# Kernel optimization log

Measured on AMD Instinct MI355X. Metric: run time of the kernel, lower is better.

## Reference

```python
import jax, jax.numpy as jnp
import numpy as np

D_MODEL = 1024
N_HEADS = 16
HEAD_DIM = D_MODEL // N_HEADS
ROPE_BASE = 10000.0


def setup_inputs() -> dict:
    key = jax.random.key(0)
    ks = jax.random.split(key, 5)
    B, S = 2, 2048
    x = jax.random.normal(ks[0], (B, S, D_MODEL), dtype=jnp.float32)
    scale = 1.0 / np.sqrt(D_MODEL)
    Wq = jax.random.normal(ks[1], (D_MODEL, D_MODEL), dtype=jnp.float32) * scale
    Wk = jax.random.normal(ks[2], (D_MODEL, D_MODEL), dtype=jnp.float32) * scale
    Wv = jax.random.normal(ks[3], (D_MODEL, D_MODEL), dtype=jnp.float32) * scale
    Wo = jax.random.normal(ks[4], (D_MODEL, D_MODEL), dtype=jnp.float32) * scale
    return {"x": x, "Wq": Wq, "Wk": Wk, "Wv": Wv, "Wo": Wo}


def _rope_cos_sin(seq_len, dtype):
    # inv_freq over half the head dim, duplicated (cat[freqs, freqs])
    inv_freq = 1.0 / (ROPE_BASE ** (jnp.arange(0, HEAD_DIM, 2, dtype=jnp.float32) / HEAD_DIM))
    t = jnp.arange(seq_len, dtype=jnp.float32)
    freqs = jnp.outer(t, inv_freq)                 # [S, HD/2]
    emb = jnp.concatenate([freqs, freqs], axis=-1)  # [S, HD]
    return jnp.cos(emb).astype(dtype), jnp.sin(emb).astype(dtype)


def _rotate_half(v):
    v1, v2 = jnp.split(v, 2, axis=-1)
    return jnp.concatenate([-v2, v1], axis=-1)


def reference(x, Wq, Wk, Wv, Wo):
    B, S, _ = x.shape
    # torch Linear: y = x @ W.T  (weights stored [out, in])
    def proj(W):
        y = jnp.einsum('bsd,ed->bse', x, W)
        return y.reshape(B, S, N_HEADS, HEAD_DIM).transpose(0, 2, 1, 3)  # [B,H,S,HD]
    q, k, v = proj(Wq), proj(Wk), proj(Wv)

    cos, sin = _rope_cos_sin(S, x.dtype)  # [S, HD]
    cos = cos[None, None]                 # [1,1,S,HD]
    sin = sin[None, None]
    q = q * cos + _rotate_half(q) * sin
    k = k * cos + _rotate_half(k) * sin

    scale = 1.0 / np.sqrt(HEAD_DIM)
    scores = jnp.einsum('bhqd,bhkd->bhqk', q, k) * scale  # [B,H,S,S]
    causal = jnp.triu(jnp.ones((S, S), dtype=bool), k=1)
    scores = jnp.where(causal, jnp.finfo(scores.dtype).min, scores)
    attn = jax.nn.softmax(scores, axis=-1)
    out = jnp.einsum('bhqk,bhkd->bhqd', attn, v)          # [B,H,S,HD]
    out = out.transpose(0, 2, 1, 3).reshape(B, S, D_MODEL)
    return jnp.einsum('bsd,ed->bse', out, Wo)
```

## Files before the change

### kernel.cpp

```cpp
#include <hip/hip_runtime.h>

typedef unsigned short u16;
typedef __attribute__((ext_vector_type(8))) short short8;
typedef __attribute__((ext_vector_type(4))) float floatx4;

#define D_MODEL 1024
#define NHEADS 16
#define HD 64
#define BATCH 2
#define SEQ 2048
#define MROWS (BATCH * SEQ)

static __device__ __forceinline__ u16 f2bf(float f) {
  unsigned int u = __float_as_uint(f);
  u += 0x7fffu + ((u >> 16) & 1u);
  return (u16)(u >> 16);
}

__global__ void cvt_all(const float* __restrict__ x, const float* __restrict__ wq,
                        const float* __restrict__ wk, const float* __restrict__ wv,
                        const float* __restrict__ wo, u16* __restrict__ xb,
                        u16* __restrict__ wqkvb, u16* __restrict__ wob) {
  const int i = blockIdx.x * 256 + threadIdx.x;
  const int chunk = i >> 18;
  const float* src;
  u16* dst;
  int loc;
  switch (chunk) {
    case 0: case 1: case 2: case 3: src = x;  dst = xb;              loc = i;              break;
    case 4:                          src = wq; dst = wqkvb;           loc = i - (4 << 18); break;
    case 5:                          src = wk; dst = wqkvb + 1048576; loc = i - (5 << 18); break;
    case 6:                          src = wv; dst = wqkvb + 2097152; loc = i - (6 << 18); break;
    default:                         src = wo; dst = wob;             loc = i - (7 << 18); break;
  }
  const float4 v = ((const float4*)src)[loc];
  ushort4 o;
  o.x = f2bf(v.x); o.y = f2bf(v.y); o.z = f2bf(v.z); o.w = f2bf(v.w);
  ((ushort4*)dst)[loc] = o;
}

__global__ __launch_bounds__(256) void gemm_qkv(
    const u16* __restrict__ A, const u16* __restrict__ B,
    u16* __restrict__ qb, u16* __restrict__ kb, u16* __restrict__ vb, int K) {
  __shared__ u16 As[128 * 32];
  __shared__ u16 Bs[128 * 32];
  const int t = threadIdx.x;
  const int lane = t & 63;
  const int wv = t >> 6;
  const int wr = wv >> 1, wc = wv & 1;
  const int m0 = blockIdx.y * 128, n0 = blockIdx.x * 128;
  const int qd = lane >> 4, lr = lane & 15;
  const int arow = lane >> 2;
  const int acol = (lane & 3) * 8;

  floatx4 acc[4][4];
#pragma unroll
  for (int i = 0; i < 4; ++i)
#pragma unroll
    for (int j = 0; j < 4; ++j) acc[i][j] = (floatx4){0.f, 0.f, 0.f, 0.f};

  for (int kt = 0; kt < K; kt += 32) {
    __syncthreads();
#pragma unroll
    for (int i = 0; i < 2; ++i) {
      const int seg = wv * 2 + i;
      const u16* ga = &A[(size_t)(m0 + seg * 16 + arow) * K + kt + acol];
      const u16* gb = &B[(size_t)(n0 + seg * 16 + arow) * K + kt + acol];
      __builtin_amdgcn_global_load_lds(
          (const __attribute__((address_space(1))) void*)ga,
          (__attribute__((address_space(3))) void*)&As[seg * 512], 16, 0, 0);
      __builtin_amdgcn_global_load_lds(
          (const __attribute__((address_space(1))) void*)gb,
          (__attribute__((address_space(3))) void*)&Bs[seg * 512], 16, 0, 0);
    }
    __syncthreads();

    short8 af[4], bfr[4];
#pragma unroll
    for (int i = 0; i < 4; ++i)
      af[i] = *(const short8*)&As[(wr * 64 + i * 16 + lr) * 32 + qd * 8];
#pragma unroll
    for (int j = 0; j < 4; ++j)
      bfr[j] = *(const short8*)&Bs[(wc * 64 + j * 16 + lr) * 32 + qd * 8];
#pragma unroll
    for (int i = 0; i < 4; ++i)
#pragma unroll
      for (int j = 0; j < 4; ++j)
        acc[i][j] = __builtin_amdgcn_mfma_f32_16x16x32_bf16(af[i], bfr[j], acc[i][j], 0, 0, 0);
  }

  const int tn = n0 >> 10;
  if (tn == 2) {
#pragma unroll
    for (int i = 0; i < 4; ++i) {
      const int mb = m0 + wr * 64 + i * 16 + qd * 4;
      const int b = mb >> 11, s = mb & 2047;
#pragma unroll
      for (int j = 0; j < 4; ++j) {
        const int nn = (n0 + wc * 64 + j * 16 + lr) & 1023;
        const int h = nn >> 6, d = nn & 63;
        ushort4 o;
        o.x = f2bf(acc[i][j][0]); o.y = f2bf(acc[i][j][1]);
        o.z = f2bf(acc[i][j][2]); o.w = f2bf(acc[i][j][3]);
        *(ushort4*)&vb[((size_t)(b * NHEADS + h) * HD + d) * SEQ + s] = o;
      }
    }
  } else {
    u16* dst = (tn == 0) ? qb : kb;
    const float qs = (tn == 0) ? 0.18033688011112042f : 1.0f;
    const int h = ((n0 & 1023) >> 6) + wc;
    const float inv0 = __builtin_exp2f(-(float)lr * 0.4152410118609203f);
    const float inv1 = __builtin_exp2f(-(float)(lr + 16) * 0.4152410118609203f);
#pragma unroll
    for (int i = 0; i < 4; ++i) {
      const int mb = m0 + wr * 64 + i * 16 + qd * 4;
      const int b = mb >> 11;
      const size_t rowbase = (size_t)(b * NHEADS + h) * SEQ;
#pragma unroll
      for (int r = 0; r < 4; ++r) {
        const int sq = (mb + r) & 2047;
        float s0, c0, s1, c1;
        __sincosf((float)sq * inv0, &s0, &c0);
        __sincosf((float)sq * inv1, &s1, &c1);
#pragma unroll
        for (int j = 0; j < 4; ++j) {
          const float v = acc[i][j][r];
          const float pv = acc[i][j ^ 2][r];
          const float cc = (j & 1) ? c1 : c0;
          const float ss = (j & 1) ? s1 : s0;
          const float res = (v * cc + ((j < 2) ? -pv : pv) * ss) * qs;
          dst[(rowbase + sq) * HD + j * 16 + lr] = f2bf(res);
        }
      }
    }
  }
}

__global__ __launch_bounds__(256) void gemm_out(
    const u16* __restrict__ A, const u16* __restrict__ B, float* __restrict__ fo,
    int N, int K) {
  __shared__ u16 As[64 * 32];
  __shared__ u16 Bs[128 * 32];
  const int t = threadIdx.x;
  const int lane = t & 63, wv = t >> 6;
  const int m0 = blockIdx.y * 64, n0 = blockIdx.x * 128;
  const int qd = lane >> 4, lr = lane & 15;
  const int arow = lane >> 2;
  const int acol = (lane & 3) * 8;

  floatx4 acc[8];
#pragma unroll
  for (int j = 0; j < 8; ++j) acc[j] = (floatx4){0.f, 0.f, 0.f, 0.f};

  for (int kt = 0; kt < K; kt += 32) {
    __syncthreads();
    {
      const u16* ga = &A[(size_t)(m0 + wv * 16 + arow) * K + kt + acol];
      __builtin_amdgcn_global_load_lds(
          (const __attribute__((address_space(1))) void*)ga,
          (__attribute__((address_space(3))) void*)&As[wv * 512], 16, 0, 0);
#pragma unroll
      for (int i = 0; i < 2; ++i) {
        const int seg = wv * 2 + i;
        const u16* gb = &B[(size_t)(n0 + seg * 16 + arow) * K + kt + acol];
        __builtin_amdgcn_global_load_lds(
            (const __attribute__((address_space(1))) void*)gb,
            (__attribute__((address_space(3))) void*)&Bs[seg * 512], 16, 0, 0);
      }
    }
    __syncthreads();
    const short8 af = *(const short8*)&As[(wv * 16 + lr) * 32 + qd * 8];
#pragma unroll
    for (int j = 0; j < 8; ++j) {
      const short8 bfr = *(const short8*)&Bs[(j * 16 + lr) * 32 + qd * 8];
      acc[j] = __builtin_amdgcn_mfma_f32_16x16x32_bf16(af, bfr, acc[j], 0, 0, 0);
    }
  }
#pragma unroll
  for (int j = 0; j < 8; ++j)
#pragma unroll
    for (int r = 0; r < 4; ++r)
      fo[(size_t)(m0 + wv * 16 + qd * 4 + r) * N + n0 + j * 16 + lr] = acc[j][r];
}

__global__ __launch_bounds__(256, 2) void flash_mfma(
    const u16* __restrict__ Q, const u16* __restrict__ Kg,
    const u16* __restrict__ Vg, u16* __restrict__ O) {
  __shared__ u16 Ks[2][2][64 * 32];
  __shared__ u16 Vs[2][2][64 * 32];
  __shared__ u16 Ps[4][2][16][72];
  const int t = threadIdx.x;
  const int lane = t & 63, wv = t >> 6;
  const int lr = lane & 15, qd = lane >> 4;
  const int bh = blockIdx.x;
  const int y = (int)blockIdx.y;
  const int c = (y < 8) ? (15 - y) : (y - 8);
  const int nsteps = 2 * c + 2;
  const int q0w = c * 128 + wv * 32;
  const size_t baseQK = (size_t)bh * SEQ * HD;
  const size_t baseV = (size_t)bh * HD * SEQ;
  const int b = bh >> 4, h = bh & 15;
  const int srow = lane >> 2;
  const int scol = (lane & 3) * 8;

  auto stage = [&](int buf, int k0) {
    const int hh = wv & 1;
    if (wv < 2) {
#pragma unroll
      for (int seg = 0; seg < 4; ++seg) {
        const u16* g = &Kg[baseQK + (size_t)(k0 + seg * 16 + srow) * HD + hh * 32 + scol];
        __builtin_amdgcn_global_load_lds(
            (const __attribute__((address_space(1))) void*)g,
            (__attribute__((address_space(3))) void*)&Ks[buf][hh][seg * 512], 16, 0, 0);
      }
    } else {
#pragma unroll
      for (int seg = 0; seg < 4; ++seg) {
        const u16* g = &Vg[baseV + (size_t)(seg * 16 + srow) * SEQ + k0 + hh * 32 + scol];
        __builtin_amdgcn_global_load_lds(
            (const __attribute__((address_space(1))) void*)g,
            (__attribute__((address_space(3))) void*)&Vs[buf][hh][seg * 512], 16, 0, 0);
      }
    }
  };

  short8 qf[2][2];
#pragma unroll
  for (int i = 0; i < 2; ++i)
#pragma unroll
    for (int s = 0; s < 2; ++s)
      qf[i][s] = *(const short8*)&Q[baseQK + (size_t)(q0w + i * 16 + lr) * HD + s * 32 + qd * 8];

  float l_i[2] = {0.f, 0.f};
  floatx4 oacc[2][4];
#pragma unroll
  for (int i = 0; i < 2; ++i)
#pragma unroll
    for (int dj = 0; dj < 4; ++dj) oacc[i][dj] = (floatx4){0.f, 0.f, 0.f, 0.f};

  stage(0, 0);

  for (int kt = 0; kt < nsteps; ++kt) {
    __syncthreads();
    if (kt + 1 < nsteps) stage((kt + 1) & 1, (kt + 1) * 64);
    const int k0 = kt * 64;
    if (k0 > q0w + 31) continue;
    const int buf = kt & 1;

    short8 kf[2][4], vf[2][4];
#pragma unroll
    for (int s = 0; s < 2; ++s)
#pragma unroll
      for (int jj = 0; jj < 4; ++jj)
        kf[s][jj] = *(const short8*)&Ks[buf][s][(jj * 16 + lr) * 32 + qd * 8];
#pragma unroll
    for (int s = 0; s < 2; ++s)
#pragma unroll
      for (int dj = 0; dj < 4; ++dj)
        vf[s][dj] = *(const short8*)&Vs[buf][s][(dj * 16 + lr) * 32 + qd * 8];

    floatx4 sv[2][4];
#pragma unroll
    for (int i = 0; i < 2; ++i)
#pragma unroll
      for (int jj = 0; jj < 4; ++jj) sv[i][jj] = (floatx4){0.f, 0.f, 0.f, 0.f};
#pragma unroll
    for (int s = 0; s < 2; ++s)
#pragma unroll
      for (int jj = 0; jj < 4; ++jj) {
        sv[1][jj] = __builtin_amdgcn_mfma_f32_16x16x32_bf16(kf[s][jj], qf[1][s], sv[1][jj], 0, 0, 0);
        sv[0][jj] = __builtin_amdgcn_mfma_f32_16x16x32_bf16(kf[s][jj], qf[0][s], sv[0][jj], 0, 0, 0);
      }

#pragma unroll
    for (int i = 0; i < 2; ++i) {
      const int dq = (q0w + i * 16) - k0;
      if (dq < 63) {
#pragma unroll
        for (int jj = 0; jj < 4; ++jj)
#pragma unroll
          for (int r = 0; r < 4; ++r)
            if (jj * 16 + qd * 4 + r > dq + lr) sv[i][jj][r] = -1e30f;
      }
      float rs = 0.f;
#pragma unroll
      for (int jj = 0; jj < 4; ++jj) {
        const float p0 = __builtin_exp2f(sv[i][jj][0]);
        const float p1 = __builtin_exp2f(sv[i][jj][1]);
        const float p2 = __builtin_exp2f(sv[i][jj][2]);
        const float p3 = __builtin_exp2f(sv[i][jj][3]);
        rs += (p0 + p1) + (p2 + p3);
        uint2 pk;
        pk.x = __builtin_amdgcn_perm(__float_as_uint(p1), __float_as_uint(p0), 0x07060302);
        pk.y = __builtin_amdgcn_perm(__float_as_uint(p3), __float_as_uint(p2), 0x07060302);
        *(uint2*)&Ps[wv][i][lr][jj * 16 + qd * 4] = pk;
      }
      l_i[i] += rs;
    }

#pragma unroll
    for (int i = 0; i < 2; ++i) {
      const short8 pf0 = *(const short8*)&Ps[wv][i][lr][qd * 8];
      const short8 pf1 = *(const short8*)&Ps[wv][i][lr][32 + qd * 8];
#pragma unroll
      for (int dj = 0; dj < 4; ++dj)
        oacc[i][dj] = __builtin_amdgcn_mfma_f32_16x16x32_bf16(pf0, vf[0][dj], oacc[i][dj], 0, 0, 0);
#pragma unroll
      for (int dj = 0; dj < 4; ++dj)
        oacc[i][dj] = __builtin_amdgcn_mfma_f32_16x16x32_bf16(pf1, vf[1][dj], oacc[i][dj], 0, 0, 0);
    }
  }

#pragma unroll
  for (int i = 0; i < 2; ++i) {
    float lf = l_i[i];
    lf += __shfl_xor(lf, 16, 64);
    lf += __shfl_xor(lf, 32, 64);
#pragma unroll
    for (int r = 0; r < 4; ++r) {
      const float linv = 1.f / __shfl(lf, qd * 4 + r, 64);
      const int q = q0w + i * 16 + qd * 4 + r;
#pragma unroll
      for (int dj = 0; dj < 4; ++dj)
        O[(size_t)(b * SEQ + q) * D_MODEL + h * HD + dj * 16 + lr] = f2bf(oacc[i][dj][r] * linv);
    }
  }
}

extern "C" void kernel_launch(void* const* d_in, const int* in_sizes, int n_in,
                              void* d_out, int out_size, void* d_ws, size_t ws_size,
                              hipStream_t stream) {
  const float* x  = (const float*)d_in[0];
  const float* Wq = (const float*)d_in[1];
  const float* Wk = (const float*)d_in[2];
  const float* Wv = (const float*)d_in[3];
  const float* Wo = (const float*)d_in[4];
  float* out = (float*)d_out;

  u16* xb = (u16*)d_ws;
  u16* wqkv = xb + 4194304;
  u16* wo = wqkv + 3145728;
  u16* qb = wo + 1048576;
  u16* kb = qb + 4194304;
  u16* vb = kb + 4194304;
  u16* ow = vb + 4194304;

  cvt_all<<<8192, 256, 0, stream>>>(x, Wq, Wk, Wv, Wo, xb, wqkv, wo);
  gemm_qkv<<<dim3(24, 32), 256, 0, stream>>>(xb, wqkv, qb, kb, vb, 1024);
  flash_mfma<<<dim3(32, 16), 256, 0, stream>>>(qb, kb, vb, ow);
  gemm_out<<<dim3(8, 64), 256, 0, stream>>>(ow, wo, out, 1024, 1024);
}
```

Measured before the change: 186.6 us.

## Fuse all stages into one persistent kernel with atomic grid barriers

```diff
diff --git a/kernel.cpp b/kernel.cpp
--- a/kernel.cpp
+++ b/kernel.cpp
@@ -9,7 +9,7 @@
 #define HD 64
 #define BATCH 2
 #define SEQ 2048
-#define MROWS (BATCH * SEQ)
+#define NBLK 512u
 
 static __device__ __forceinline__ u16 f2bf(float f) {
   unsigned int u = __float_as_uint(f);
@@ -17,313 +17,318 @@
   return (u16)(u >> 16);
 }
 
-__global__ void cvt_all(const float* __restrict__ x, const float* __restrict__ wq,
-                        const float* __restrict__ wk, const float* __restrict__ wv,
-                        const float* __restrict__ wo, u16* __restrict__ xb,
-                        u16* __restrict__ wqkvb, u16* __restrict__ wob) {
-  const int i = blockIdx.x * 256 + threadIdx.x;
-  const int chunk = i >> 18;
-  const float* src;
-  u16* dst;
-  int loc;
-  switch (chunk) {
-    case 0: case 1: case 2: case 3: src = x;  dst = xb;              loc = i;              break;
-    case 4:                          src = wq; dst = wqkvb;           loc = i - (4 << 18); break;
-    case 5:                          src = wk; dst = wqkvb + 1048576; loc = i - (5 << 18); break;
-    case 6:                          src = wv; dst = wqkvb + 2097152; loc = i - (6 << 18); break;
-    default:                         src = wo; dst = wob;             loc = i - (7 << 18); break;
-  }
-  const float4 v = ((const float4*)src)[loc];
-  ushort4 o;
-  o.x = f2bf(v.x); o.y = f2bf(v.y); o.z = f2bf(v.z); o.w = f2bf(v.w);
-  ((ushort4*)dst)[loc] = o;
-}
-
-__global__ __launch_bounds__(256) void gemm_qkv(
-    const u16* __restrict__ A, const u16* __restrict__ B,
-    u16* __restrict__ qb, u16* __restrict__ kb, u16* __restrict__ vb, int K) {
-  __shared__ u16 As[128 * 32];
-  __shared__ u16 Bs[128 * 32];
-  const int t = threadIdx.x;
-  const int lane = t & 63;
-  const int wv = t >> 6;
-  const int wr = wv >> 1, wc = wv & 1;
-  const int m0 = blockIdx.y * 128, n0 = blockIdx.x * 128;
-  const int qd = lane >> 4, lr = lane & 15;
-  const int arow = lane >> 2;
-  const int acol = (lane & 3) * 8;
-
-  floatx4 acc[4][4];
-#pragma unroll
-  for (int i = 0; i < 4; ++i)
-#pragma unroll
-    for (int j = 0; j < 4; ++j) acc[i][j] = (floatx4){0.f, 0.f, 0.f, 0.f};
-
-  for (int kt = 0; kt < K; kt += 32) {
-    __syncthreads();
-#pragma unroll
-    for (int i = 0; i < 2; ++i) {
-      const int seg = wv * 2 + i;
-      const u16* ga = &A[(size_t)(m0 + seg * 16 + arow) * K + kt + acol];
-      const u16* gb = &B[(size_t)(n0 + seg * 16 + arow) * K + kt + acol];
-      __builtin_amdgcn_global_load_lds(
-          (const __attribute__((address_space(1))) void*)ga,
-          (__attribute__((address_space(3))) void*)&As[seg * 512], 16, 0, 0);
-      __builtin_amdgcn_global_load_lds(
-          (const __attribute__((address_space(1))) void*)gb,
-          (__attribute__((address_space(3))) void*)&Bs[seg * 512], 16, 0, 0);
-    }
-    __syncthreads();
-
-    short8 af[4], bfr[4];
-#pragma unroll
-    for (int i = 0; i < 4; ++i)
-      af[i] = *(const short8*)&As[(wr * 64 + i * 16 + lr) * 32 + qd * 8];
-#pragma unroll
-    for (int j = 0; j < 4; ++j)
-      bfr[j] = *(const short8*)&Bs[(wc * 64 + j * 16 + lr) * 32 + qd * 8];
-#pragma unroll
-    for (int i = 0; i < 4; ++i)
-#pragma unroll
-      for (int j = 0; j < 4; ++j)
-        acc[i][j] = __builtin_amdgcn_mfma_f32_16x16x32_bf16(af[i], bfr[j], acc[i][j], 0, 0, 0);
-  }
-
-  const int tn = n0 >> 10;
-  if (tn == 2) {
-#pragma unroll
-    for (int i = 0; i < 4; ++i) {
-      const int mb = m0 + wr * 64 + i * 16 + qd * 4;
-      const int b = mb >> 11, s = mb & 2047;
-#pragma unroll
-      for (int j = 0; j < 4; ++j) {
-        const int nn = (n0 + wc * 64 + j * 16 + lr) & 1023;
-        const int h = nn >> 6, d = nn & 63;
-        ushort4 o;
-        o.x = f2bf(acc[i][j][0]); o.y = f2bf(acc[i][j][1]);
-        o.z = f2bf(acc[i][j][2]); o.w = f2bf(acc[i][j][3]);
-        *(ushort4*)&vb[((size_t)(b * NHEADS + h) * HD + d) * SEQ + s] = o;
-      }
-    }
-  } else {
-    u16* dst = (tn == 0) ? qb : kb;
-    const float qs = (tn == 0) ? 0.18033688011112042f : 1.0f;
-    const int h = ((n0 & 1023) >> 6) + wc;
-    const float inv0 = __builtin_exp2f(-(float)lr * 0.4152410118609203f);
-    const float inv1 = __builtin_exp2f(-(float)(lr + 16) * 0.4152410118609203f);
-#pragma unroll
-    for (int i = 0; i < 4; ++i) {
-      const int mb = m0 + wr * 64 + i * 16 + qd * 4;
-      const int b = mb >> 11;
-      const size_t rowbase = (size_t)(b * NHEADS + h) * SEQ;
-#pragma unroll
-      for (int r = 0; r < 4; ++r) {
-        const int sq = (mb + r) & 2047;
-        float s0, c0, s1, c1;
-        __sincosf((float)sq * inv0, &s0, &c0);
-        __sincosf((float)sq * inv1, &s1, &c1);
-#pragma unroll
-        for (int j = 0; j < 4; ++j) {
-          const float v = acc[i][j][r];
-          const float pv = acc[i][j ^ 2][r];
-          const float cc = (j & 1) ? c1 : c0;
-          const float ss = (j & 1) ? s1 : s0;
-          const float res = (v * cc + ((j < 2) ? -pv : pv) * ss) * qs;
-          dst[(rowbase + sq) * HD + j * 16 + lr] = f2bf(res);
-        }
-      }
-    }
-  }
-}
-
-__global__ __launch_bounds__(256) void gemm_out(
-    const u16* __restrict__ A, const u16* __restrict__ B, float* __restrict__ fo,
-    int N, int K) {
-  __shared__ u16 As[64 * 32];
-  __shared__ u16 Bs[128 * 32];
-  const int t = threadIdx.x;
-  const int lane = t & 63, wv = t >> 6;
-  const int m0 = blockIdx.y * 64, n0 = blockIdx.x * 128;
-  const int qd = lane >> 4, lr = lane & 15;
-  const int arow = lane >> 2;
-  const int acol = (lane & 3) * 8;
-
-  floatx4 acc[8];
-#pragma unroll
-  for (int j = 0; j < 8; ++j) acc[j] = (floatx4){0.f, 0.f, 0.f, 0.f};
-
-  for (int kt = 0; kt < K; kt += 32) {
-    __syncthreads();
-    {
-      const u16* ga = &A[(size_t)(m0 + wv * 16 + arow) * K + kt + acol];
-      __builtin_amdgcn_global_load_lds(
-          (const __attribute__((address_space(1))) void*)ga,
-          (__attribute__((address_space(3))) void*)&As[wv * 512], 16, 0, 0);
-#pragma unroll
-      for (int i = 0; i < 2; ++i) {
-        const int seg = wv * 2 + i;
-        const u16* gb = &B[(size_t)(n0 + seg * 16 + arow) * K + kt + acol];
-        __builtin_amdgcn_global_load_lds(
-            (const __attribute__((address_space(1))) void*)gb,
-            (__attribute__((address_space(3))) void*)&Bs[seg * 512], 16, 0, 0);
-      }
-    }
-    __syncthreads();
-    const short8 af = *(const short8*)&As[(wv * 16 + lr) * 32 + qd * 8];
-#pragma unroll
-    for (int j = 0; j < 8; ++j) {
-      const short8 bfr = *(const short8*)&Bs[(j * 16 + lr) * 32 + qd * 8];
-      acc[j] = __builtin_amdgcn_mfma_f32_16x16x32_bf16(af, bfr, acc[j], 0, 0, 0);
-    }
-  }
-#pragma unroll
-  for (int j = 0; j < 8; ++j)
-#pragma unroll
-    for (int r = 0; r < 4; ++r)
-      fo[(size_t)(m0 + wv * 16 + qd * 4 + r) * N + n0 + j * 16 + lr] = acc[j][r];
-}
-
-__global__ __launch_bounds__(256, 2) void flash_mfma(
-    const u16* __restrict__ Q, const u16* __restrict__ Kg,
-    const u16* __restrict__ Vg, u16* __restrict__ O) {
-  __shared__ u16 Ks[2][2][64 * 32];
-  __shared__ u16 Vs[2][2][64 * 32];
-  __shared__ u16 Ps[4][2][16][72];
+static __device__ __forceinline__ void glds16(const u16* g, u16* l) {
+  __builtin_amdgcn_global_load_lds(
+      (const __attribute__((address_space(1))) void*)g,
+      (__attribute__((address_space(3))) void*)l, 16, 0, 0);
+}
+
+static __device__ __forceinline__ void grid_barrier(unsigned* ctr) {
+  __syncthreads();
+  if (threadIdx.x == 0) {
+    __threadfence();
+    __hip_atomic_fetch_add(ctr, 1u, __ATOMIC_ACQ_REL, __HIP_MEMORY_SCOPE_AGENT);
+    while (__hip_atomic_load(ctr, __ATOMIC_ACQUIRE, __HIP_MEMORY_SCOPE_AGENT) < NBLK)
+      __builtin_amdgcn_s_sleep(8);
+    __threadfence();
+  }
+  __syncthreads();
+}
+
+__global__ void init_ctr(unsigned* ctr) {
+  if (threadIdx.x < 4) ctr[threadIdx.x] = 0u;
+}
+
+__global__ __launch_bounds__(256, 2) void fused_mha(
+    const float* __restrict__ x, const float* __restrict__ Wq,
+    const float* __restrict__ Wk, const float* __restrict__ Wv,
+    const float* __restrict__ Wo, float* __restrict__ out,
+    u16* __restrict__ xb, u16* __restrict__ wqkv, u16* __restrict__ wo,
+    u16* __restrict__ qb, u16* __restrict__ kb, u16* __restrict__ vb,
+    u16* __restrict__ ow, unsigned* __restrict__ ctr) {
+  __shared__ __align__(16) char smem_raw[51200];
+  const int bid = blockIdx.x;
   const int t = threadIdx.x;
   const int lane = t & 63, wv = t >> 6;
   const int lr = lane & 15, qd = lane >> 4;
-  const int bh = blockIdx.x;
-  const int y = (int)blockIdx.y;
-  const int c = (y < 8) ? (15 - y) : (y - 8);
-  const int nsteps = 2 * c + 2;
-  const int q0w = c * 128 + wv * 32;
-  const size_t baseQK = (size_t)bh * SEQ * HD;
-  const size_t baseV = (size_t)bh * HD * SEQ;
-  const int b = bh >> 4, h = bh & 15;
-  const int srow = lane >> 2;
-  const int scol = (lane & 3) * 8;
-
-  auto stage = [&](int buf, int k0) {
-    const int hh = wv & 1;
-    if (wv < 2) {
-#pragma unroll
-      for (int seg = 0; seg < 4; ++seg) {
-        const u16* g = &Kg[baseQK + (size_t)(k0 + seg * 16 + srow) * HD + hh * 32 + scol];
-        __builtin_amdgcn_global_load_lds(
-            (const __attribute__((address_space(1))) void*)g,
-            (__attribute__((address_space(3))) void*)&Ks[buf][hh][seg * 512], 16, 0, 0);
-      }
-    } else {
-#pragma unroll
-      for (int seg = 0; seg < 4; ++seg) {
-        const u16* g = &Vg[baseV + (size_t)(seg * 16 + srow) * SEQ + k0 + hh * 32 + scol];
-        __builtin_amdgcn_global_load_lds(
-            (const __attribute__((address_space(1))) void*)g,
-            (__attribute__((address_space(3))) void*)&Vs[buf][hh][seg * 512], 16, 0, 0);
-      }
-    }
-  };
-
-  short8 qf[2][2];
-#pragma unroll
-  for (int i = 0; i < 2; ++i)
-#pragma unroll
-    for (int s = 0; s < 2; ++s)
-      qf[i][s] = *(const short8*)&Q[baseQK + (size_t)(q0w + i * 16 + lr) * HD + s * 32 + qd * 8];
-
-  float l_i[2] = {0.f, 0.f};
-  floatx4 oacc[2][4];
-#pragma unroll
-  for (int i = 0; i < 2; ++i)
-#pragma unroll
-    for (int dj = 0; dj < 4; ++dj) oacc[i][dj] = (floatx4){0.f, 0.f, 0.f, 0.f};
-
-  stage(0, 0);
-
-  for (int kt = 0; kt < nsteps; ++kt) {
-    __syncthreads();
-    if (kt + 1 < nsteps) stage((kt + 1) & 1, (kt + 1) * 64);
-    const int k0 = kt * 64;
-    if (k0 > q0w + 31) continue;
-    const int buf = kt & 1;
-
-    short8 kf[2][4], vf[2][4];
-#pragma unroll
-    for (int s = 0; s < 2; ++s)
-#pragma unroll
-      for (int jj = 0; jj < 4; ++jj)
-        kf[s][jj] = *(const short8*)&Ks[buf][s][(jj * 16 + lr) * 32 + qd * 8];
-#pragma unroll
-    for (int s = 0; s < 2; ++s)
-#pragma unroll
-      for (int dj = 0; dj < 4; ++dj)
-        vf[s][dj] = *(const short8*)&Vs[buf][s][(dj * 16 + lr) * 32 + qd * 8];
-
-    floatx4 sv[2][4];
+  const int arow = lane >> 2;
+  const int acol = (lane & 3) * 8;
+
+  {
+#pragma unroll
+    for (int s = 0; s < 16; ++s) {
+      const int i = bid * 256 + t + s * 131072;
+      const int chunk = i >> 18;
+      const float* src;
+      u16* dst;
+      int loc;
+      switch (chunk) {
+        case 0: case 1: case 2: case 3: src = x;  dst = xb;             loc = i;             break;
+        case 4:                         src = Wq; dst = wqkv;           loc = i - (4 << 18); break;
+        case 5:                         src = Wk; dst = wqkv + 1048576; loc = i - (5 << 18); break;
+        case 6:                         src = Wv; dst = wqkv + 2097152; loc = i - (6 << 18); break;
+        default:                        src = Wo; dst = wo;             loc = i - (7 << 18); break;
+      }
+      const float4 v = ((const float4*)src)[loc];
+      ushort4 o;
+      o.x = f2bf(v.x); o.y = f2bf(v.y); o.z = f2bf(v.z); o.w = f2bf(v.w);
+      ((ushort4*)dst)[loc] = o;
+    }
+  }
+  grid_barrier(&ctr[0]);
+
+  {
+    u16* As = (u16*)smem_raw;
+    u16* Bs = (u16*)(smem_raw + 16384);
+    for (int tt = 0; tt < 3; ++tt) {
+      const int tile = bid + (tt << 9);
+      const int nx = tile >> 6, my = tile & 63;
+      const int m0 = my * 64, n0 = nx * 128;
+
+      floatx4 acc[8];
+#pragma unroll
+      for (int j = 0; j < 8; ++j) acc[j] = (floatx4){0.f, 0.f, 0.f, 0.f};
+
+      for (int kt = 0; kt < 1024; kt += 64) {
+        __syncthreads();
+#pragma unroll
+        for (int kh = 0; kh < 2; ++kh) {
+          glds16(&xb[(size_t)(m0 + wv * 16 + arow) * 1024 + kt + kh * 32 + acol],
+                 &As[kh * 2048 + wv * 512]);
+#pragma unroll
+          for (int i2 = 0; i2 < 2; ++i2) {
+            const int seg = wv * 2 + i2;
+            glds16(&wqkv[(size_t)(n0 + seg * 16 + arow) * 1024 + kt + kh * 32 + acol],
+                   &Bs[kh * 4096 + seg * 512]);
+          }
+        }
+        __syncthreads();
+#pragma unroll
+        for (int kh = 0; kh < 2; ++kh) {
+          const short8 af = *(const short8*)&As[kh * 2048 + (wv * 16 + lr) * 32 + qd * 8];
+#pragma unroll
+          for (int j = 0; j < 8; ++j) {
+            const short8 bfr = *(const short8*)&Bs[kh * 4096 + (j * 16 + lr) * 32 + qd * 8];
+            acc[j] = __builtin_amdgcn_mfma_f32_16x16x32_bf16(af, bfr, acc[j], 0, 0, 0);
+          }
+        }
+      }
+
+      const int tn = n0 >> 10;
+      const int mb = m0 + wv * 16 + qd * 4;
+      const int b = mb >> 11;
+      if (tn == 2) {
+        const int s = mb & 2047;
+#pragma unroll
+        for (int j = 0; j < 8; ++j) {
+          const int nn = (n0 + j * 16 + lr) & 1023;
+          const int h = nn >> 6, d = nn & 63;
+          ushort4 o;
+          o.x = f2bf(acc[j][0]); o.y = f2bf(acc[j][1]);
+          o.z = f2bf(acc[j][2]); o.w = f2bf(acc[j][3]);
+          *(ushort4*)&vb[((size_t)(b * NHEADS + h) * HD + d) * SEQ + s] = o;
+        }
+      } else {
+        u16* dst = (tn == 0) ? qb : kb;
+        const float qs = (tn == 0) ? 0.18033688011112042f : 1.0f;
+        const int hb = (n0 & 1023) >> 6;
+        const float inv0 = __builtin_exp2f(-(float)lr * 0.4152410118609203f);
+        const float inv1 = __builtin_exp2f(-(float)(lr + 16) * 0.4152410118609203f);
+#pragma unroll
+        for (int r = 0; r < 4; ++r) {
+          const int sq = (mb + r) & 2047;
+          float s0, c0, s1, c1;
+          __sincosf((float)sq * inv0, &s0, &c0);
+          __sincosf((float)sq * inv1, &s1, &c1);
+#pragma unroll
+          for (int j = 0; j < 8; ++j) {
+            const float v = acc[j][r];
+            const float pv = acc[j ^ 2][r];
+            const float cc = (j & 1) ? c1 : c0;
+            const float ss = (j & 1) ? s1 : s0;
+            const float res = (v * cc + ((j & 2) ? pv : -pv) * ss) * qs;
+            const int h = hb + (j >> 2);
+            dst[((size_t)(b * NHEADS + h) * SEQ + sq) * HD + (j & 3) * 16 + lr] = f2bf(res);
+          }
+        }
+      }
+    }
+  }
+  grid_barrier(&ctr[1]);
+
+  {
+    u16* KsP = (u16*)smem_raw;
+    u16* VsP = (u16*)(smem_raw + 16384);
+    u16* PsP = (u16*)(smem_raw + 32768);
+    const int bh = bid & 31;
+    const int y = bid >> 5;
+    const int c = (y < 8) ? (15 - y) : (y - 8);
+    const int nsteps = 2 * c + 2;
+    const int q0w = c * 128 + wv * 32;
+    const size_t baseQK = (size_t)bh * SEQ * HD;
+    const size_t baseV = (size_t)bh * HD * SEQ;
+    const int b = bh >> 4, h = bh & 15;
+    const int srow = lane >> 2;
+    const int scol = (lane & 3) * 8;
+
+    short8 qf[2][2];
 #pragma unroll
     for (int i = 0; i < 2; ++i)
 #pragma unroll
-      for (int jj = 0; jj < 4; ++jj) sv[i][jj] = (floatx4){0.f, 0.f, 0.f, 0.f};
-#pragma unroll
-    for (int s = 0; s < 2; ++s)
-#pragma unroll
-      for (int jj = 0; jj < 4; ++jj) {
-        sv[1][jj] = __builtin_amdgcn_mfma_f32_16x16x32_bf16(kf[s][jj], qf[1][s], sv[1][jj], 0, 0, 0);
-        sv[0][jj] = __builtin_amdgcn_mfma_f32_16x16x32_bf16(kf[s][jj], qf[0][s], sv[0][jj], 0, 0, 0);
-      }
+      for (int s = 0; s < 2; ++s)
+        qf[i][s] = *(const short8*)&qb[baseQK + (size_t)(q0w + i * 16 + lr) * HD + s * 32 + qd * 8];
+
+    float l_i[2] = {0.f, 0.f};
+    floatx4 oacc[2][4];
+#pragma unroll
+    for (int i = 0; i < 2; ++i)
+#pragma unroll
+      for (int dj = 0; dj < 4; ++dj) oacc[i][dj] = (floatx4){0.f, 0.f, 0.f, 0.f};
+
+    auto stage = [&](int buf, int k0) {
+      const int hh = wv & 1;
+      if (wv < 2) {
+#pragma unroll
+        for (int seg = 0; seg < 4; ++seg)
+          glds16(&kb[baseQK + (size_t)(k0 + seg * 16 + srow) * HD + hh * 32 + scol],
+                 &KsP[(buf * 2 + hh) * 2048 + seg * 512]);
+      } else {
+#pragma unroll
+        for (int seg = 0; seg < 4; ++seg)
+          glds16(&vb[baseV + (size_t)(seg * 16 + srow) * SEQ + k0 + hh * 32 + scol],
+                 &VsP[(buf * 2 + hh) * 2048 + seg * 512]);
+      }
+    };
+
+    stage(0, 0);
+
+    for (int kt = 0; kt < nsteps; ++kt) {
+      __syncthreads();
+      if (kt + 1 < nsteps) stage((kt + 1) & 1, (kt + 1) * 64);
+      const int k0 = kt * 64;
+      if (k0 > q0w + 31) continue;
+      const int buf = kt & 1;
+
+      short8 kf[2][4], vf[2][4];
+#pragma unroll
+      for (int s = 0; s < 2; ++s)
+#pragma unroll
+        for (int jj = 0; jj < 4; ++jj)
+          kf[s][jj] = *(const short8*)&KsP[(buf * 2 + s) * 2048 + (jj * 16 + lr) * 32 + qd * 8];
+#pragma unroll
+      for (int s = 0; s < 2; ++s)
+#pragma unroll
+        for (int dj = 0; dj < 4; ++dj)
+          vf[s][dj] = *(const short8*)&VsP[(buf * 2 + s) * 2048 + (dj * 16 + lr) * 32 + qd * 8];
+
+      floatx4 sv[2][4];
+#pragma unroll
+      for (int i = 0; i < 2; ++i)
+#pragma unroll
+        for (int jj = 0; jj < 4; ++jj) sv[i][jj] = (floatx4){0.f, 0.f, 0.f, 0.f};
+#pragma unroll
+      for (int s = 0; s < 2; ++s)
+#pragma unroll
+        for (int jj = 0; jj < 4; ++jj) {
+          sv[1][jj] = __builtin_amdgcn_mfma_f32_16x16x32_bf16(kf[s][jj], qf[1][s], sv[1][jj], 0, 0, 0);
+          sv[0][jj] = __builtin_amdgcn_mfma_f32_16x16x32_bf16(kf[s][jj], qf[0][s], sv[0][jj], 0, 0, 0);
+        }
+
+#pragma unroll
+      for (int i = 0; i < 2; ++i) {
+        const int dq = (q0w + i * 16) - k0;
+        if (dq < 63) {
+#pragma unroll
+          for (int jj = 0; jj < 4; ++jj)
+#pragma unroll
+            for (int r = 0; r < 4; ++r)
+              if (jj * 16 + qd * 4 + r > dq + lr) sv[i][jj][r] = -1e30f;
+        }
+        float rs = 0.f;
+#pragma unroll
+        for (int jj = 0; jj < 4; ++jj) {
+          const float p0 = __builtin_exp2f(sv[i][jj][0]);
+          const float p1 = __builtin_exp2f(sv[i][jj][1]);
+          const float p2 = __builtin_exp2f(sv[i][jj][2]);
+          const float p3 = __builtin_exp2f(sv[i][jj][3]);
+          rs += (p0 + p1) + (p2 + p3);
+          uint2 pk;
+          pk.x = __builtin_amdgcn_perm(__float_as_uint(p1), __float_as_uint(p0), 0x07060302);
+          pk.y = __builtin_amdgcn_perm(__float_as_uint(p3), __float_as_uint(p2), 0x07060302);
+          *(uint2*)&PsP[((wv * 2 + i) * 16 + lr) * 72 + jj * 16 + qd * 4] = pk;
+        }
+        l_i[i] += rs;
+      }
+
+#pragma unroll
+      for (int i = 0; i < 2; ++i) {
+        const short8 pf0 = *(const short8*)&PsP[((wv * 2 + i) * 16 + lr) * 72 + qd * 8];
+        const short8 pf1 = *(const short8*)&PsP[((wv * 2 + i) * 16 + lr) * 72 + 32 + qd * 8];
+#pragma unroll
+        for (int dj = 0; dj < 4; ++dj)
+          oacc[i][dj] = __builtin_amdgcn_mfma_f32_16x16x32_bf16(pf0, vf[0][dj], oacc[i][dj], 0, 0, 0);
+#pragma unroll
+        for (int dj = 0; dj < 4; ++dj)
+          oacc[i][dj] = __builtin_amdgcn_mfma_f32_16x16x32_bf16(pf1, vf[1][dj], oacc[i][dj], 0, 0, 0);
+      }
+    }
 
 #pragma unroll
     for (int i = 0; i < 2; ++i) {
-      const int dq = (q0w + i * 16) - k0;
-      if (dq < 63) {
-#pragma unroll
-        for (int jj = 0; jj < 4; ++jj)
-#pragma unroll
-          for (int r = 0; r < 4; ++r)
-            if (jj * 16 + qd * 4 + r > dq + lr) sv[i][jj][r] = -1e30f;
-      }
-      float rs = 0.f;
-#pragma unroll
-      for (int jj = 0; jj < 4; ++jj) {
-        const float p0 = __builtin_exp2f(sv[i][jj][0]);
-        const float p1 = __builtin_exp2f(sv[i][jj][1]);
-        const float p2 = __builtin_exp2f(sv[i][jj][2]);
-        const float p3 = __builtin_exp2f(sv[i][jj][3]);
-        rs += (p0 + p1) + (p2 + p3);
-        uint2 pk;
-        pk.x = __builtin_amdgcn_perm(__float_as_uint(p1), __float_as_uint(p0), 0x07060302);
-        pk.y = __builtin_amdgcn_perm(__float_as_uint(p3), __float_as_uint(p2), 0x07060302);
-        *(uint2*)&Ps[wv][i][lr][jj * 16 + qd * 4] = pk;
-      }
-      l_i[i] += rs;
-    }
-
-#pragma unroll
-    for (int i = 0; i < 2; ++i) {
-      const short8 pf0 = *(const short8*)&Ps[wv][i][lr][qd * 8];
-      const short8 pf1 = *(const short8*)&Ps[wv][i][lr][32 + qd * 8];
-#pragma unroll
-      for (int dj = 0; dj < 4; ++dj)
-        oacc[i][dj] = __builtin_amdgcn_mfma_f32_16x16x32_bf16(pf0, vf[0][dj], oacc[i][dj], 0, 0, 0);
-#pragma unroll
-      for (int dj = 0; dj < 4; ++dj)
-        oacc[i][dj] = __builtin_amdgcn_mfma_f32_16x16x32_bf16(pf1, vf[1][dj], oacc[i][dj], 0, 0, 0);
-    }
-  }
-
-#pragma unroll
-  for (int i = 0; i < 2; ++i) {
-    float lf = l_i[i];
-    lf += __shfl_xor(lf, 16, 64);
-    lf += __shfl_xor(lf, 32, 64);
-#pragma unroll
-    for (int r = 0; r < 4; ++r) {
-      const float linv = 1.f / __shfl(lf, qd * 4 + r, 64);
-      const int q = q0w + i * 16 + qd * 4 + r;
-#pragma unroll
-      for (int dj = 0; dj < 4; ++dj)
-        O[(size_t)(b * SEQ + q) * D_MODEL + h * HD + dj * 16 + lr] = f2bf(oacc[i][dj][r] * linv);
-    }
+      float lf = l_i[i];
+      lf += __shfl_xor(lf, 16, 64);
+      lf += __shfl_xor(lf, 32, 64);
+#pragma unroll
+      for (int r = 0; r < 4; ++r) {
+        const float linv = 1.f / __shfl(lf, qd * 4 + r, 64);
+        const int q = q0w + i * 16 + qd * 4 + r;
+#pragma unroll
+        for (int dj = 0; dj < 4; ++dj)
+          ow[(size_t)(b * SEQ + q) * D_MODEL + h * HD + dj * 16 + lr] = f2bf(oacc[i][dj][r] * linv);
+      }
+    }
+  }
+  grid_barrier(&ctr[2]);
+
+  {
+    u16* As = (u16*)smem_raw;
+    u16* Bs = (u16*)(smem_raw + 16384);
+    const int nx = bid >> 6, my = bid & 63;
+    const int m0 = my * 64, n0 = nx * 128;
+
+    floatx4 acc[8];
+#pragma unroll
+    for (int j = 0; j < 8; ++j) acc[j] = (floatx4){0.f, 0.f, 0.f, 0.f};
+
+    for (int kt = 0; kt < 1024; kt += 64) {
+      __syncthreads();
+#pragma unroll
+      for (int kh = 0; kh < 2; ++kh) {
+        glds16(&ow[(size_t)(m0 + wv * 16 + arow) * 1024 + kt + kh * 32 + acol],
+               &As[kh * 2048 + wv * 512]);
+#pragma unroll
+        for (int i2 = 0; i2 < 2; ++i2) {
+          const int seg = wv * 2 + i2;
+          glds16(&wo[(size_t)(n0 + seg * 16 + arow) * 1024 + kt + kh * 32 + acol],
+                 &Bs[kh * 4096 + seg * 512]);
+        }
+      }
+      __syncthreads();
+#pragma unroll
+      for (int kh = 0; kh < 2; ++kh) {
+        const short8 af = *(const short8*)&As[kh * 2048 + (wv * 16 + lr) * 32 + qd * 8];
+#pragma unroll
+        for (int j = 0; j < 8; ++j) {
+          const short8 bfr = *(const short8*)&Bs[kh * 4096 + (j * 16 + lr) * 32 + qd * 8];
+          acc[j] = __builtin_amdgcn_mfma_f32_16x16x32_bf16(af, bfr, acc[j], 0, 0, 0);
+        }
+      }
+    }
+#pragma unroll
+    for (int j = 0; j < 8; ++j)
+#pragma unroll
+      for (int r = 0; r < 4; ++r)
+        out[(size_t)(m0 + wv * 16 + qd * 4 + r) * 1024 + n0 + j * 16 + lr] = acc[j][r];
   }
 }
 
@@ -344,9 +349,10 @@
   u16* kb = qb + 4194304;
   u16* vb = kb + 4194304;
   u16* ow = vb + 4194304;
-
-  cvt_all<<<8192, 256, 0, stream>>>(x, Wq, Wk, Wv, Wo, xb, wqkv, wo);
-  gemm_qkv<<<dim3(24, 32), 256, 0, stream>>>(xb, wqkv, qb, kb, vb, 1024);
-  flash_mfma<<<dim3(32, 16), 256, 0, stream>>>(qb, kb, vb, ow);
-  gemm_out<<<dim3(8, 64), 256, 0, stream>>>(ow, wo, out, 1024, 1024);
-}
+  unsigned* ctr = (unsigned*)(ow + 4194304);
+
+  init_ctr<<<1, 64, 0, stream>>>(ctr);
+  void* dummy = nullptr; (void)dummy;
+  fused_mha<<<NBLK, 256, 0, stream>>>(x, Wq, Wk, Wv, Wo, out, xb, wqkv, wo,
+                                      qb, kb, vb, ow, ctr);
+}
```

Result: slower. 453.6 us (+143.1%).
